# Performance work log

Measured on AMD Instinct MI355X. Metric: run time of the kernel, lower is better.

## Reference

```python
import jax, jax.numpy as jnp
import numpy as np

EPS = 1e-6  # torch.nn.PairwiseDistance default eps, added to the difference


def _supinf(c1, c2):
    # c1: [B, L1, D], c2: [B, L2, D]
    # directed Hausdorff: max over points in c2 of min dist to c1
    diff = c2[:, :, None, :] - c1[:, None, :, :] + EPS  # [B, L2, L1, D]
    dist = jnp.sqrt(jnp.sum(diff * diff, axis=-1))       # [B, L2, L1]
    return jnp.max(jnp.min(dist, axis=2), axis=1)        # [B]


def setup_inputs() -> dict:
    key = jax.random.key(0)
    k1, k2, k3 = jax.random.split(key, 3)
    B, L1, L2, D = 8, 4096, 4096, 2
    return {
        "contour1": jax.random.normal(k1, (B, L1, D), dtype=jnp.float32),
        "contour2": jax.random.normal(k2, (B, L2, D), dtype=jnp.float32),
        "resolution": jax.random.uniform(k3, (B,), dtype=jnp.float32),
    }


def reference(contour1, contour2, resolution):
    h21 = _supinf(contour1, contour2)  # sup over contour2 of inf dist to contour1
    h12 = _supinf(contour2, contour1)  # sup over contour1 of inf dist to contour2
    return jnp.maximum(h12, h21) * resolution  # [B]
```

## Files before the change

### kernel.cpp

```cpp
#include <hip/hip_runtime.h>
#include <hip/hip_bf16.h>
#include <float.h>

#define EPSV 1e-6f
#define SRC_BLK 128
#define NFRAG 4
#define LT_MAX 4096
#define WAVES 8

typedef float  f32x16_t __attribute__((ext_vector_type(16)));
typedef short  bf16x8_t __attribute__((ext_vector_type(8)));
typedef unsigned short u16;
typedef u16    u16x8    __attribute__((ext_vector_type(8)));

__device__ __forceinline__ u16 bf_hi(float v) {
    return __bfloat16_as_ushort(__float2bfloat16(v));
}
__device__ __forceinline__ float bf_f(u16 u) {
    return __bfloat162float(__ushort_as_bfloat16(u));
}

__global__ __launch_bounds__(512, 2) void hausdorff_mfma_kernel(
    const float* __restrict__ c1, const float* __restrict__ c2,
    float* __restrict__ ws, int L1, int L2, int STmax) {

    const int b   = blockIdx.y;
    const int B   = gridDim.y;
    const int dir = blockIdx.z;
    const int st  = blockIdx.x;

    const float* src; const float* tgt; int Lsrc, Ltgt;
    if (dir == 0) { src = c2 + (size_t)b * L2 * 2; tgt = c1 + (size_t)b * L1 * 2; Lsrc = L2; Ltgt = L1; }
    else          { src = c1 + (size_t)b * L1 * 2; tgt = c2 + (size_t)b * L2 * 2; Lsrc = L1; Ltgt = L2; }

    const int srcBase = st * SRC_BLK;
    if (srcBase >= Lsrc) return;

    const int lane = threadIdx.x & 63;
    const int w    = threadIdx.x >> 6;

    __shared__ u16x8 Tform[LT_MAX];
    __shared__ u16x8 Sform[SRC_BLK];
    __shared__ u16x8 zslot;
    __shared__ float s2s[SRC_BLK];
    __shared__ float red[WAVES][SRC_BLK];
    __shared__ float rmax[2];

    if (threadIdx.x < SRC_BLK) {
        const int j = srcBase + threadIdx.x;
        float sx = 0.f, sy = 0.f;
        const bool ok = (j < Lsrc);
        if (ok) {
            float2 p = ((const float2*)src)[j];
            sx = p.x + EPSV; sy = p.y + EPSV;
        }
        const float nx = -2.0f * sx, ny = -2.0f * sy;
        const u16 nxh = bf_hi(nx); const u16 nxl = bf_hi(nx - bf_f(nxh));
        const u16 nyh = bf_hi(ny); const u16 nyl = bf_hi(ny - bf_f(nyh));
        const u16 one = bf_hi(1.0f);
        u16x8 r;
        r[0] = nxh; r[1] = nxh; r[2] = nxl;
        r[3] = nyh; r[4] = nyh; r[5] = nyl;
        r[6] = one; r[7] = one;
        Sform[threadIdx.x] = r;
        s2s[threadIdx.x] = ok ? fmaf(sx, sx, sy * sy) : -FLT_MAX;
    }
    if (threadIdx.x == 128) {
        zslot = (u16x8){0, 0, 0, 0, 0, 0, 0, 0};
    }
    __syncthreads();

    bf16x8_t bfrag[NFRAG];
    #pragma unroll
    for (int f = 0; f < NFRAG; ++f) {
        const bf16x8_t* bp = (lane < 32)
            ? &((const bf16x8_t*)Sform)[f * 32 + lane]
            : (const bf16x8_t*)&zslot;
        bfrag[f] = *bp;
    }

    float mm[NFRAG];
    #pragma unroll
    for (int f = 0; f < NFRAG; ++f) mm[f] = FLT_MAX;

    const f32x16_t zacc = {0.f,0.f,0.f,0.f, 0.f,0.f,0.f,0.f,
                           0.f,0.f,0.f,0.f, 0.f,0.f,0.f,0.f};
    const u16 padhi = bf_hi(1e30f);

    for (int tbase = 0; tbase < Ltgt; tbase += LT_MAX) {
        const int chunk  = min(LT_MAX, Ltgt - tbase);
        const int padded = (chunk + 31) & ~31;

        for (int e = threadIdx.x; e < padded; e += 512) {
            u16x8 r;
            if (e < chunk) {
                float2 p = ((const float2*)tgt)[tbase + e];
                const float t2 = fmaf(p.y, p.y, p.x * p.x);
                const u16 txh = bf_hi(p.x); const u16 txl = bf_hi(p.x - bf_f(txh));
                const u16 tyh = bf_hi(p.y); const u16 tyl = bf_hi(p.y - bf_f(tyh));
                const u16 t2h = bf_hi(t2);  const u16 t2l = bf_hi(t2 - bf_f(t2h));
                r[0] = txh; r[1] = txl; r[2] = txh;
                r[3] = tyh; r[4] = tyl; r[5] = tyh;
                r[6] = t2h; r[7] = t2l;
            } else {
                r = (u16x8){0, 0, 0, 0, 0, 0, 0, 0};
                r[6] = padhi;
            }
            Tform[e] = r;
        }
        __syncthreads();

        const int ntile = padded >> 5;
        const int tbeg  = (w * ntile) >> 3;
        const int tend  = ((w + 1) * ntile) >> 3;

        if (tbeg < tend) {
            const bf16x8_t* Ap = (const bf16x8_t*)Tform;
            bf16x8_t af = Ap[tbeg * 32 + (lane & 31)];
            for (int t = tbeg; t < tend; ++t) {
                const int tn = (t + 1 < tend) ? t + 1 : t;
                bf16x8_t afn = Ap[tn * 32 + (lane & 31)];
                #pragma unroll
                for (int f = 0; f < NFRAG; ++f) {
                    f32x16_t acc = __builtin_amdgcn_mfma_f32_32x32x16_bf16(
                        af, bfrag[f], zacc, 0, 0, 0);
                    mm[f] = fminf(fminf(mm[f], acc[0]),  acc[1]);
                    mm[f] = fminf(fminf(mm[f], acc[2]),  acc[3]);
                    mm[f] = fminf(fminf(mm[f], acc[4]),  acc[5]);
                    mm[f] = fminf(fminf(mm[f], acc[6]),  acc[7]);
                    mm[f] = fminf(fminf(mm[f], acc[8]),  acc[9]);
                    mm[f] = fminf(fminf(mm[f], acc[10]), acc[11]);
                    mm[f] = fminf(fminf(mm[f], acc[12]), acc[13]);
                    mm[f] = fminf(fminf(mm[f], acc[14]), acc[15]);
                }
                af = afn;
            }
        }
        __syncthreads();
    }

    #pragma unroll
    for (int f = 0; f < NFRAG; ++f) {
        float v = mm[f];
        v = fminf(v, __shfl_xor(v, 32));
        if (lane < 32) red[w][f * 32 + lane] = v;
    }
    __syncthreads();

    const int t = threadIdx.x;
    float v = 0.f;
    if (t < SRC_BLK) {
        float m = red[0][t];
        #pragma unroll
        for (int ww = 1; ww < WAVES; ++ww) m = fminf(m, red[ww][t]);
        v = fmaxf(s2s[t] + m, 0.f);
    }
    for (int off = 32; off > 0; off >>= 1)
        v = fmaxf(v, __shfl_down(v, off));
    if (t < SRC_BLK && lane == 0) rmax[t >> 6] = v;
    __syncthreads();
    if (t == 0) {
        ws[(size_t)(dir * B + b) * STmax + st] = fmaxf(rmax[0], rmax[1]);
    }
}

__global__ void hausdorff_finalize_kernel(
    const float* __restrict__ ws, const float* __restrict__ res,
    float* __restrict__ out, int STmax, int nst0, int nst1, int B) {

    const int b = blockIdx.x;
    const int lane = threadIdx.x;
    float v = 0.f;
    for (int i = lane; i < nst0 + nst1; i += 64) {
        v = fmaxf(v, (i < nst0) ? ws[(size_t)(0 * B + b) * STmax + i]
                                : ws[(size_t)(1 * B + b) * STmax + (i - nst0)]);
    }
    for (int off = 32; off > 0; off >>= 1)
        v = fmaxf(v, __shfl_down(v, off));
    if (lane == 0) out[b] = sqrtf(v) * res[b];
}

extern "C" void kernel_launch(void* const* d_in, const int* in_sizes, int n_in,
                              void* d_out, int out_size, void* d_ws, size_t ws_size,
                              hipStream_t stream) {
    const float* c1  = (const float*)d_in[0];
    const float* c2  = (const float*)d_in[1];
    const float* res = (const float*)d_in[2];
    float* out = (float*)d_out;

    const int B  = in_sizes[2];
    const int L1 = in_sizes[0] / (B * 2);
    const int L2 = in_sizes[1] / (B * 2);

    float* ws = (float*)d_ws;

    const int Lmax  = max(L1, L2);
    const int STmax = (Lmax + SRC_BLK - 1) / SRC_BLK;
    const int nst0  = (L2 + SRC_BLK - 1) / SRC_BLK;
    const int nst1  = (L1 + SRC_BLK - 1) / SRC_BLK;

    dim3 gridA(STmax, B, 2);
    hipLaunchKernelGGL(hausdorff_mfma_kernel, gridA, dim3(512), 0, stream,
                       c1, c2, ws, L1, L2, STmax);

    hipLaunchKernelGGL(hausdorff_finalize_kernel, dim3(B), dim3(64), 0, stream,
                       ws, res, out, STmax, nst0, nst1, B);
}
```

Baseline: 17.65 us.

## Load target points directly from global memory per wave, dropping LDS staging

The 64KB LDS staging buffer for target points and its barrier are gone. Each wave now loads its own target tiles straight from global memory, two tiles ahead, and converts them into split-bf16 MFMA operands in registers. The per-tile min reduction becomes a tree instead of a serial chain, and a zero register replaces the zero slot in LDS. The smaller LDS footprint can allow more blocks per CU, but every wave now repeats the bf16 split arithmetic for each tile, and those global loads sit on the MFMA critical path.

```diff
diff --git a/kernel.cpp b/kernel.cpp
--- a/kernel.cpp
+++ b/kernel.cpp
@@ -5,7 +5,6 @@
 #define EPSV 1e-6f
 #define SRC_BLK 128
 #define NFRAG 4
-#define LT_MAX 4096
 #define WAVES 8
 
 typedef float  f32x16_t __attribute__((ext_vector_type(16)));
@@ -38,10 +37,9 @@
 
     const int lane = threadIdx.x & 63;
     const int w    = threadIdx.x >> 6;
-
-    __shared__ u16x8 Tform[LT_MAX];
+    const int rlane = lane & 31;
+
     __shared__ u16x8 Sform[SRC_BLK];
-    __shared__ u16x8 zslot;
     __shared__ float s2s[SRC_BLK];
     __shared__ float red[WAVES][SRC_BLK];
     __shared__ float rmax[2];
@@ -65,18 +63,13 @@
         Sform[threadIdx.x] = r;
         s2s[threadIdx.x] = ok ? fmaf(sx, sx, sy * sy) : -FLT_MAX;
     }
-    if (threadIdx.x == 128) {
-        zslot = (u16x8){0, 0, 0, 0, 0, 0, 0, 0};
-    }
     __syncthreads();
 
+    const bf16x8_t z8 = (bf16x8_t){0, 0, 0, 0, 0, 0, 0, 0};
     bf16x8_t bfrag[NFRAG];
     #pragma unroll
     for (int f = 0; f < NFRAG; ++f) {
-        const bf16x8_t* bp = (lane < 32)
-            ? &((const bf16x8_t*)Sform)[f * 32 + lane]
-            : (const bf16x8_t*)&zslot;
-        bfrag[f] = *bp;
+        bfrag[f] = (lane < 32) ? ((const bf16x8_t*)Sform)[f * 32 + lane] : z8;
     }
 
     float mm[NFRAG];
@@ -87,57 +80,60 @@
                            0.f,0.f,0.f,0.f, 0.f,0.f,0.f,0.f};
     const u16 padhi = bf_hi(1e30f);
 
-    for (int tbase = 0; tbase < Ltgt; tbase += LT_MAX) {
-        const int chunk  = min(LT_MAX, Ltgt - tbase);
-        const int padded = (chunk + 31) & ~31;
-
-        for (int e = threadIdx.x; e < padded; e += 512) {
-            u16x8 r;
-            if (e < chunk) {
-                float2 p = ((const float2*)tgt)[tbase + e];
-                const float t2 = fmaf(p.y, p.y, p.x * p.x);
-                const u16 txh = bf_hi(p.x); const u16 txl = bf_hi(p.x - bf_f(txh));
-                const u16 tyh = bf_hi(p.y); const u16 tyl = bf_hi(p.y - bf_f(tyh));
-                const u16 t2h = bf_hi(t2);  const u16 t2l = bf_hi(t2 - bf_f(t2h));
-                r[0] = txh; r[1] = txl; r[2] = txh;
-                r[3] = tyh; r[4] = tyl; r[5] = tyh;
-                r[6] = t2h; r[7] = t2l;
-            } else {
-                r = (u16x8){0, 0, 0, 0, 0, 0, 0, 0};
-                r[6] = padhi;
-            }
-            Tform[e] = r;
-        }
-        __syncthreads();
-
-        const int ntile = padded >> 5;
-        const int tbeg  = (w * ntile) >> 3;
-        const int tend  = ((w + 1) * ntile) >> 3;
-
-        if (tbeg < tend) {
-            const bf16x8_t* Ap = (const bf16x8_t*)Tform;
-            bf16x8_t af = Ap[tbeg * 32 + (lane & 31)];
-            for (int t = tbeg; t < tend; ++t) {
-                const int tn = (t + 1 < tend) ? t + 1 : t;
-                bf16x8_t afn = Ap[tn * 32 + (lane & 31)];
-                #pragma unroll
-                for (int f = 0; f < NFRAG; ++f) {
-                    f32x16_t acc = __builtin_amdgcn_mfma_f32_32x32x16_bf16(
-                        af, bfrag[f], zacc, 0, 0, 0);
-                    mm[f] = fminf(fminf(mm[f], acc[0]),  acc[1]);
-                    mm[f] = fminf(fminf(mm[f], acc[2]),  acc[3]);
-                    mm[f] = fminf(fminf(mm[f], acc[4]),  acc[5]);
-                    mm[f] = fminf(fminf(mm[f], acc[6]),  acc[7]);
-                    mm[f] = fminf(fminf(mm[f], acc[8]),  acc[9]);
-                    mm[f] = fminf(fminf(mm[f], acc[10]), acc[11]);
-                    mm[f] = fminf(fminf(mm[f], acc[12]), acc[13]);
-                    mm[f] = fminf(fminf(mm[f], acc[14]), acc[15]);
-                }
-                af = afn;
+    const int ntile = (Ltgt + 31) >> 5;
+    const int tbeg  = (w * ntile) >> 3;
+    const int tend  = ((w + 1) * ntile) >> 3;
+    const float2* tg = (const float2*)tgt;
+
+#define LOADT(t, pv, okv) {                                        \
+        const int row_ = (t) * 32 + rlane;                         \
+        okv = (row_ < Ltgt);                                       \
+        pv  = tg[okv ? row_ : (Ltgt - 1)]; }
+
+#define CONV(pv, okv, af) {                                                  \
+        const float t2_ = fmaf((pv).y, (pv).y, (pv).x * (pv).x);             \
+        u16 txh = bf_hi((pv).x); u16 txl = bf_hi((pv).x - bf_f(txh));        \
+        u16 tyh = bf_hi((pv).y); u16 tyl = bf_hi((pv).y - bf_f(tyh));        \
+        u16 t2h = bf_hi(t2_);    u16 t2l = bf_hi(t2_ - bf_f(t2h));           \
+        if (!(okv)) { txh = txl = tyh = tyl = 0; t2h = padhi; t2l = 0; }     \
+        u16x8 rr;                                                            \
+        rr[0] = txh; rr[1] = txl; rr[2] = txh;                               \
+        rr[3] = tyh; rr[4] = tyl; rr[5] = tyh;                               \
+        rr[6] = t2h; rr[7] = t2l;                                            \
+        af = *(bf16x8_t*)&rr; }
+
+    if (tbeg < tend) {
+        float2 pa, pb; bool va, vb;
+        LOADT(tbeg, pa, va);
+        pb = pa; vb = va;
+        if (tbeg + 1 < tend) { LOADT(tbeg + 1, pb, vb); }
+        for (int t = tbeg; t < tend; ++t) {
+            const float2 pc = pa; const bool vc = va;
+            pa = pb; va = vb;
+            if (t + 2 < tend) { LOADT(t + 2, pb, vb); }
+            bf16x8_t af;
+            CONV(pc, vc, af);
+            #pragma unroll
+            for (int f = 0; f < NFRAG; ++f) {
+                f32x16_t acc = __builtin_amdgcn_mfma_f32_32x32x16_bf16(
+                    af, bfrag[f], zacc, 0, 0, 0);
+                float a0 = fminf(acc[0],  acc[1]);
+                float a1 = fminf(acc[2],  acc[3]);
+                float a2 = fminf(acc[4],  acc[5]);
+                float a3 = fminf(acc[6],  acc[7]);
+                float a4 = fminf(acc[8],  acc[9]);
+                float a5 = fminf(acc[10], acc[11]);
+                float a6 = fminf(acc[12], acc[13]);
+                float a7 = fminf(acc[14], acc[15]);
+                a0 = fminf(a0, a1); a2 = fminf(a2, a3);
+                a4 = fminf(a4, a5); a6 = fminf(a6, a7);
+                a0 = fminf(a0, a2); a4 = fminf(a4, a6);
+                mm[f] = fminf(mm[f], fminf(a0, a4));
             }
         }
-        __syncthreads();
-    }
+    }
+#undef LOADT
+#undef CONV
 
     #pragma unroll
     for (int f = 0; f < NFRAG; ++f) {
```

Result: slower. 25.36 us (+43.7%).

## Software-pipeline MFMA tiles with ping-pong accumulators and tree min-reduction

Applied to the files above, without the earlier changes.

The inner loop is restructured so that the MFMAs for the next target tile are issued while the min-reduction of the previous tile's accumulators runs, using two sets of accumulator registers (a and b). The serial fminf chain is replaced with a shallower tree reduction. The zero-padding LDS slot is replaced by a register constant. Launch bounds are relaxed to one block per CU, which frees registers for the doubled accumulators but may lower occupancy.

```diff
diff --git a/kernel.cpp b/kernel.cpp
--- a/kernel.cpp
+++ b/kernel.cpp
@@ -20,7 +20,7 @@
     return __bfloat162float(__ushort_as_bfloat16(u));
 }
 
-__global__ __launch_bounds__(512, 2) void hausdorff_mfma_kernel(
+__global__ __launch_bounds__(512, 1) void hausdorff_mfma_kernel(
     const float* __restrict__ c1, const float* __restrict__ c2,
     float* __restrict__ ws, int L1, int L2, int STmax) {
 
@@ -36,12 +36,12 @@
     const int srcBase = st * SRC_BLK;
     if (srcBase >= Lsrc) return;
 
-    const int lane = threadIdx.x & 63;
-    const int w    = threadIdx.x >> 6;
+    const int lane  = threadIdx.x & 63;
+    const int w     = threadIdx.x >> 6;
+    const int rlane = lane & 31;
 
     __shared__ u16x8 Tform[LT_MAX];
     __shared__ u16x8 Sform[SRC_BLK];
-    __shared__ u16x8 zslot;
     __shared__ float s2s[SRC_BLK];
     __shared__ float red[WAVES][SRC_BLK];
     __shared__ float rmax[2];
@@ -65,18 +65,13 @@
         Sform[threadIdx.x] = r;
         s2s[threadIdx.x] = ok ? fmaf(sx, sx, sy * sy) : -FLT_MAX;
     }
-    if (threadIdx.x == 128) {
-        zslot = (u16x8){0, 0, 0, 0, 0, 0, 0, 0};
-    }
     __syncthreads();
 
+    const bf16x8_t z8 = (bf16x8_t){0, 0, 0, 0, 0, 0, 0, 0};
     bf16x8_t bfrag[NFRAG];
     #pragma unroll
     for (int f = 0; f < NFRAG; ++f) {
-        const bf16x8_t* bp = (lane < 32)
-            ? &((const bf16x8_t*)Sform)[f * 32 + lane]
-            : (const bf16x8_t*)&zslot;
-        bfrag[f] = *bp;
+        bfrag[f] = (lane < 32) ? ((const bf16x8_t*)Sform)[f * 32 + lane] : z8;
     }
 
     float mm[NFRAG];
@@ -86,6 +81,22 @@
     const f32x16_t zacc = {0.f,0.f,0.f,0.f, 0.f,0.f,0.f,0.f,
                            0.f,0.f,0.f,0.f, 0.f,0.f,0.f,0.f};
     const u16 padhi = bf_hi(1e30f);
+
+#define RED(acc, f) {                                                       \
+        float q0 = fminf(fminf((acc)[0],  (acc)[1]),  (acc)[2]);            \
+        float q1 = fminf(fminf((acc)[3],  (acc)[4]),  (acc)[5]);            \
+        float q2 = fminf(fminf((acc)[6],  (acc)[7]),  (acc)[8]);            \
+        float q3 = fminf(fminf((acc)[9],  (acc)[10]), (acc)[11]);           \
+        float q4 = fminf(fminf((acc)[12], (acc)[13]), (acc)[14]);           \
+        q0 = fminf(fminf(q0, q1), q2);                                      \
+        q3 = fminf(fminf(q3, q4), (acc)[15]);                               \
+        mm[f] = fminf(fminf(mm[f], q0), q3); }
+
+#define MFMA4(dst0, dst1, dst2, dst3, af)                                   \
+        dst0 = __builtin_amdgcn_mfma_f32_32x32x16_bf16(af, bfrag[0], zacc, 0, 0, 0); \
+        dst1 = __builtin_amdgcn_mfma_f32_32x32x16_bf16(af, bfrag[1], zacc, 0, 0, 0); \
+        dst2 = __builtin_amdgcn_mfma_f32_32x32x16_bf16(af, bfrag[2], zacc, 0, 0, 0); \
+        dst3 = __builtin_amdgcn_mfma_f32_32x32x16_bf16(af, bfrag[3], zacc, 0, 0, 0);
 
     for (int tbase = 0; tbase < Ltgt; tbase += LT_MAX) {
         const int chunk  = min(LT_MAX, Ltgt - tbase);
@@ -116,28 +127,33 @@
 
         if (tbeg < tend) {
             const bf16x8_t* Ap = (const bf16x8_t*)Tform;
-            bf16x8_t af = Ap[tbeg * 32 + (lane & 31)];
-            for (int t = tbeg; t < tend; ++t) {
-                const int tn = (t + 1 < tend) ? t + 1 : t;
-                bf16x8_t afn = Ap[tn * 32 + (lane & 31)];
-                #pragma unroll
-                for (int f = 0; f < NFRAG; ++f) {
-                    f32x16_t acc = __builtin_amdgcn_mfma_f32_32x32x16_bf16(
-                        af, bfrag[f], zacc, 0, 0, 0);
-                    mm[f] = fminf(fminf(mm[f], acc[0]),  acc[1]);
-                    mm[f] = fminf(fminf(mm[f], acc[2]),  acc[3]);
-                    mm[f] = fminf(fminf(mm[f], acc[4]),  acc[5]);
-                    mm[f] = fminf(fminf(mm[f], acc[6]),  acc[7]);
-                    mm[f] = fminf(fminf(mm[f], acc[8]),  acc[9]);
-                    mm[f] = fminf(fminf(mm[f], acc[10]), acc[11]);
-                    mm[f] = fminf(fminf(mm[f], acc[12]), acc[13]);
-                    mm[f] = fminf(fminf(mm[f], acc[14]), acc[15]);
-                }
-                af = afn;
+            f32x16_t a0, a1, a2, a3, b0, b1, b2, b3;
+
+            bf16x8_t afA = Ap[tbeg * 32 + rlane];
+            MFMA4(a0, a1, a2, a3, afA)
+            bf16x8_t afB = Ap[min(tbeg + 1, tend - 1) * 32 + rlane];
+
+            int t = tbeg + 1;
+            for (; t + 1 < tend; t += 2) {
+                MFMA4(b0, b1, b2, b3, afB)
+                afA = Ap[(t + 1) * 32 + rlane];
+                RED(a0, 0) RED(a1, 1) RED(a2, 2) RED(a3, 3)
+                MFMA4(a0, a1, a2, a3, afA)
+                afB = Ap[min(t + 2, tend - 1) * 32 + rlane];
+                RED(b0, 0) RED(b1, 1) RED(b2, 2) RED(b3, 3)
+            }
+            if (t < tend) {
+                MFMA4(b0, b1, b2, b3, afB)
+                RED(a0, 0) RED(a1, 1) RED(a2, 2) RED(a3, 3)
+                RED(b0, 0) RED(b1, 1) RED(b2, 2) RED(b3, 3)
+            } else {
+                RED(a0, 0) RED(a1, 1) RED(a2, 2) RED(a3, 3)
             }
         }
         __syncthreads();
     }
+#undef RED
+#undef MFMA4
 
     #pragma unroll
     for (int f = 0; f < NFRAG; ++f) {
```

New measurement: 20.15 us. +14.1%, slower.
